# Performance work log

Measured on AMD Instinct MI355X. Metric: run time of the kernel, lower is better.

Reference implementation:

```python
import jax, jax.numpy as jnp
import numpy as np

N_NODES = 12288
N_EDGES = 393216  # N_NODES * avg_degree 32
IN_DIM, H1, H2 = 1433, 32, 16


def setup_inputs() -> dict:
    key = jax.random.key(0)
    ks = jax.random.split(key, 7)

    def glorot(k, fan_in, fan_out):
        r = np.sqrt(6.0 / (fan_in + fan_out)).astype(np.float32)
        return jax.random.uniform(k, (fan_in, fan_out), jnp.float32, -r, r)

    return {
        "X": jax.random.normal(ks[0], (N_NODES, IN_DIM), jnp.float32),
        "W1": glorot(ks[1], IN_DIM, H1),
        "W2": glorot(ks[2], H1, H1),
        "W3": glorot(ks[3], H1, H2),
        "edge_val": jax.random.uniform(ks[4], (N_EDGES,), jnp.float32),
        "edge_row": jax.random.randint(ks[5], (N_EDGES,), 0, N_NODES, jnp.int32),
        "edge_col": jax.random.randint(ks[6], (N_EDGES,), 0, N_NODES, jnp.int32),
    }


def reference(X, W1, W2, W3, edge_val, edge_row, edge_col):
    n = X.shape[0]

    def spmm(x):
        # sparse adj (COO) @ x : gather source rows, scale, scatter-add to dest
        return jax.ops.segment_sum(edge_val[:, None] * x[edge_col], edge_row, num_segments=n)

    h = jax.nn.relu(spmm(X @ W1))       # [N, 32]
    h = jax.nn.relu(spmm(h @ W2))       # [N, 32]
    Z = spmm(h @ W3)                    # [N, 16] (identity activation)
    A_pred = jax.nn.sigmoid(Z @ Z.T)    # [N, N] dot-product decode
    return (A_pred, Z)
```

## Files before the change

kernel.cpp:

```cpp
#include <hip/hip_runtime.h>


constexpr int NN = 12288;
constexpr int NE = 393216;
constexpr int KD = 1433;
constexpr int CAP = 96;

typedef float f32x4 __attribute__((ext_vector_type(4)));
typedef float f32x4u __attribute__((ext_vector_type(4), aligned(4)));
typedef float f32x16 __attribute__((ext_vector_type(16)));
typedef short shortx8 __attribute__((ext_vector_type(8)));

__device__ __forceinline__ unsigned short f2bf(float v) {
    unsigned int b = __float_as_uint(v);
    return (unsigned short)((b + 0x7FFFu + ((b >> 16) & 1u)) >> 16);
}

constexpr int KC = 256;
constexpr int NCH = 6;
constexpr int XST = KC + 8;
constexpr int G1B = (NN / 64) * NCH;

__global__ __launch_bounds__(256) void k_scatter_gemm1(const int* __restrict__ er,
                                                       const int* __restrict__ ec,
                                                       const float* __restrict__ ev,
                                                       int* __restrict__ cnt,
                                                       uint2* __restrict__ ebuf,
                                                       const float* __restrict__ X,
                                                       const float* __restrict__ W,
                                                       float* __restrict__ out) {
    if (blockIdx.x >= G1B) {
        int e = (blockIdx.x - G1B) * 256 + threadIdx.x;
        int r = er[e];
        int p = atomicAdd(&cnt[r], 1);
        if (p < CAP) ebuf[(size_t)r * CAP + p] = make_uint2((unsigned)ec[e], __float_as_uint(ev[e]));
        return;
    }
    __shared__ unsigned short wt[32 * XST];

    int rgB   = blockIdx.x / NCH;
    int chunk = blockIdx.x % NCH;
    int r0 = rgB * 64;
    int k0 = chunk * KC;
    int kt = min(KC, KD - k0);
    int nm = (kt + 15) >> 4;
    int t = threadIdx.x;

    int wtot = nm * 16 * 32;
    for (int e = t; e < wtot; e += 256) {
        int k = e >> 5, c = e & 31;
        float v = (k < kt) ? W[(size_t)(k0 + k) * 32 + c] : 0.f;
        wt[c * XST + k] = f2bf(v);
    }
    __syncthreads();

    int w = t >> 6, l = t & 63;
    int rg = w >> 1;
    int lr = l & 31, lh = l >> 5;
    int row = r0 + rg * 32 + lr;
    const float* xr = X + (size_t)row * KD + k0 + lh * 8;
    const unsigned short* wbase = wt + lr * XST + lh * 8;
    f32x16 acc = {0.f};
    for (int m = (w & 1); m < nm; m += 2) {
        int kk = m * 16 + lh * 8;
        float xv[8];
        if (kk + 8 <= kt) {
            f32x4u v0 = *(const f32x4u*)(xr + m * 16);
            f32x4u v1 = *(const f32x4u*)(xr + m * 16 + 4);
#pragma unroll
            for (int j = 0; j < 4; ++j) { xv[j] = v0[j]; xv[4 + j] = v1[j]; }
        } else {
#pragma unroll
            for (int j = 0; j < 8; ++j) xv[j] = (kk + j < kt) ? xr[m * 16 + j] : 0.f;
        }
        shortx8 a;
#pragma unroll
        for (int j = 0; j < 8; ++j) a[j] = (short)f2bf(xv[j]);
        shortx8 b = *(const shortx8*)(wbase + m * 16);
        acc = __builtin_amdgcn_mfma_f32_32x32x16_bf16(a, b, acc, 0, 0, 0);
    }
#pragma unroll
    for (int q = 0; q < 16; ++q) {
        int rf = (q & 3) + 8 * (q >> 2) + 4 * lh;
        atomicAdd(&out[(size_t)(r0 + rg * 32 + rf) * 32 + lr], acc[q]);
    }
}

template <int CO>
__global__ __launch_bounds__(256) void spmm_gemm(const float* __restrict__ in,
                                                 const float* __restrict__ Wm,
                                                 float* __restrict__ out,
                                                 const int* __restrict__ cnt,
                                                 const uint2* __restrict__ ebuf) {
    int tid = blockIdx.x * 256 + threadIdx.x;
    int r = tid >> 6;
    int lane = threadIdx.x & 63;
    int c = lane & 31, half = lane >> 5;
    int co = c & (CO - 1);
    float wcol[32];
#pragma unroll
    for (int k = 0; k < 32; ++k) wcol[k] = Wm[k * CO + co];
    int deg = min(cnt[r], CAP);
    int mid = (deg >> 1) & ~1;
    int lo = half ? mid : 0;
    int hi = half ? deg : mid;
    const uint2* eb2 = ebuf + (size_t)r * CAP;
    const uint4* eb4 = (const uint4*)eb2;
    float acc = 0.f;
    int i = lo;
#pragma unroll 2
    for (; i + 4 <= hi; i += 4) {
        uint4 e01 = eb4[i >> 1], e23 = eb4[(i >> 1) + 1];
        acc += __uint_as_float(e01.y) * in[(size_t)e01.x * 32 + c];
        acc += __uint_as_float(e01.w) * in[(size_t)e01.z * 32 + c];
        acc += __uint_as_float(e23.y) * in[(size_t)e23.x * 32 + c];
        acc += __uint_as_float(e23.w) * in[(size_t)e23.z * 32 + c];
    }
    for (; i < hi; ++i) {
        uint2 e = eb2[i];
        acc += __uint_as_float(e.y) * in[(size_t)e.x * 32 + c];
    }
    float h = fmaxf(acc + __shfl_xor(acc, 32), 0.f);
    float o = 0.f;
#pragma unroll
    for (int k = 0; k < 32; ++k)
        o += __shfl(h, (lane & 32) + k) * wcol[k];
    if (half == 0 && c < CO) out[(size_t)r * CO + co] = o;
}

__global__ __launch_bounds__(256) void spmm16(const float* __restrict__ in,
                                              float* __restrict__ out,
                                              unsigned short* __restrict__ zb,
                                              const int* __restrict__ cnt,
                                              const uint2* __restrict__ ebuf) {
    int tid = blockIdx.x * 256 + threadIdx.x;
    int r = tid >> 5;
    int sub = tid & 31;
    int c = sub & 15, half = sub >> 4;
    int deg = min(cnt[r], CAP);
    int mid = (deg >> 1) & ~1;
    int lo = half ? mid : 0;
    int hi = half ? deg : mid;
    const uint2* eb2 = ebuf + (size_t)r * CAP;
    const uint4* eb4 = (const uint4*)eb2;
    float acc = 0.f;
    int i = lo;
#pragma unroll 2
    for (; i + 4 <= hi; i += 4) {
        uint4 e01 = eb4[i >> 1], e23 = eb4[(i >> 1) + 1];
        acc += __uint_as_float(e01.y) * in[(size_t)e01.x * 16 + c];
        acc += __uint_as_float(e01.w) * in[(size_t)e01.z * 16 + c];
        acc += __uint_as_float(e23.y) * in[(size_t)e23.x * 16 + c];
        acc += __uint_as_float(e23.w) * in[(size_t)e23.z * 16 + c];
    }
    for (; i < hi; ++i) {
        uint2 e = eb2[i];
        acc += __uint_as_float(e.y) * in[(size_t)e.x * 16 + c];
    }
    float sv = acc + __shfl_xor(acc, 16);
    if (half == 0) {
        out[(size_t)r * 16 + c] = sv;
        zb[(size_t)r * 16 + c] = f2bf(sv);
    }
}

__global__ __launch_bounds__(256) void decode_mfma(const unsigned short* __restrict__ Zb,
                                                   float* __restrict__ A) {
    int id = blockIdx.x;
    int f = (id & 7) * (9216 / 8) + (id >> 3);
    int bi = f / 48, bj = f % 48;
    int w = threadIdx.x >> 6;
    int l = threadIdx.x & 63;
    int R = bi * 64;
    int C = bj * 256 + w * 64;
    int lr = l & 31, lh = l >> 5;

    shortx8 a0 = *(const shortx8*)(Zb + ((size_t)(R + lr) << 4) + lh * 8);
    shortx8 a1 = *(const shortx8*)(Zb + ((size_t)(R + 32 + lr) << 4) + lh * 8);
    shortx8 b0 = *(const shortx8*)(Zb + ((size_t)(C + lr) << 4) + lh * 8);
    shortx8 b1 = *(const shortx8*)(Zb + ((size_t)(C + 32 + lr) << 4) + lh * 8);

    f32x16 acc00 = {0.f}, acc01 = {0.f}, acc10 = {0.f}, acc11 = {0.f};
    acc00 = __builtin_amdgcn_mfma_f32_32x32x16_bf16(a0, b0, acc00, 0, 0, 0);
    acc01 = __builtin_amdgcn_mfma_f32_32x32x16_bf16(a0, b1, acc01, 0, 0, 0);
    acc10 = __builtin_amdgcn_mfma_f32_32x32x16_bf16(a1, b0, acc10, 0, 0, 0);
    acc11 = __builtin_amdgcn_mfma_f32_32x32x16_bf16(a1, b1, acc11, 0, 0, 0);

#pragma unroll
    for (int q = 0; q < 16; ++q) {
        int rf = (q & 3) + 8 * (q >> 2) + 4 * lh;
        float s00 = __fdividef(1.0f, 1.0f + __expf(-acc00[q]));
        float s01 = __fdividef(1.0f, 1.0f + __expf(-acc01[q]));
        float s10 = __fdividef(1.0f, 1.0f + __expf(-acc10[q]));
        float s11 = __fdividef(1.0f, 1.0f + __expf(-acc11[q]));
        __builtin_nontemporal_store(s00, &A[(size_t)(R + rf) * NN + C + lr]);
        __builtin_nontemporal_store(s01, &A[(size_t)(R + rf) * NN + C + 32 + lr]);
        __builtin_nontemporal_store(s10, &A[(size_t)(R + 32 + rf) * NN + C + lr]);
        __builtin_nontemporal_store(s11, &A[(size_t)(R + 32 + rf) * NN + C + 32 + lr]);
    }
}

extern "C" void kernel_launch(void* const* d_in, const int* in_sizes, int n_in,
                              void* d_out, int out_size, void* d_ws, size_t ws_size,
                              hipStream_t stream) {
    const float* X  = (const float*)d_in[0];
    const float* W1 = (const float*)d_in[1];
    const float* W2 = (const float*)d_in[2];
    const float* W3 = (const float*)d_in[3];
    const float* ev = (const float*)d_in[4];
    const int*   er = (const int*)d_in[5];
    const int*   ec = (const int*)d_in[6];

    float* A = (float*)d_out;
    float* Z = A + (size_t)NN * NN;

    int*   cnt = (int*)d_ws;
    float* t1 = (float*)(cnt + NN);
    float* t2 = t1 + (size_t)NN * 32;
    float* t3 = t2 + (size_t)NN * 32;
    unsigned short* Zb = (unsigned short*)t1;

    uint2* ebuf = (uint2*)(A + (size_t)140000000);

    (void)hipMemsetAsync(cnt, 0, NN * sizeof(int) + (size_t)NN * 32 * sizeof(float), stream);

    k_scatter_gemm1<<<G1B + NE / 256, 256, 0, stream>>>(er, ec, ev, cnt, ebuf, X, W1, t1);

    spmm_gemm<32><<<NN * 64 / 256, 256, 0, stream>>>(t1, W2, t2, cnt, ebuf);
    spmm_gemm<16><<<NN * 64 / 256, 256, 0, stream>>>(t2, W3, t3, cnt, ebuf);
    spmm16<<<NN * 32 / 256, 256, 0, stream>>>(t3, Z, Zb, cnt, ebuf);

    decode_mfma<<<192 * 48, 256, 0, stream>>>(Zb, A);
}
```

Baseline: 203.4 us.

## Split K across waves in-block and reduce via LDS instead of atomics

The first GEMM now gives each block 32 rows and has its four waves each take a quarter of the 1433-wide K dimension. Partial MFMA accumulators are summed in shared memory and written out with plain stores, replacing the global float atomics. Because no atomics accumulate into t1 any more, the output no longer needs zeroing and the memset is shortened. W1 is now read straight from global memory per lane rather than staged in LDS, which risks more and less-coalesced W traffic in exchange for dropping the staging pass and sync.

```diff
diff --git a/kernel.cpp b/kernel.cpp
--- a/kernel.cpp
+++ b/kernel.cpp
@@ -16,10 +16,9 @@
     return (unsigned short)((b + 0x7FFFu + ((b >> 16) & 1u)) >> 16);
 }
 
-constexpr int KC = 256;
-constexpr int NCH = 6;
-constexpr int XST = KC + 8;
-constexpr int G1B = (NN / 64) * NCH;
+constexpr int KQ = 368;
+constexpr int NMQ = 23;
+constexpr int G1B = NN / 32;
 
 __global__ __launch_bounds__(256) void k_scatter_gemm1(const int* __restrict__ er,
                                                        const int* __restrict__ ec,
@@ -36,53 +35,50 @@
         if (p < CAP) ebuf[(size_t)r * CAP + p] = make_uint2((unsigned)ec[e], __float_as_uint(ev[e]));
         return;
     }
-    __shared__ unsigned short wt[32 * XST];
-
-    int rgB   = blockIdx.x / NCH;
-    int chunk = blockIdx.x % NCH;
-    int r0 = rgB * 64;
-    int k0 = chunk * KC;
-    int kt = min(KC, KD - k0);
-    int nm = (kt + 15) >> 4;
+    __shared__ float cbuf[4][32 * 32];
+
+    int r0 = blockIdx.x * 32;
     int t = threadIdx.x;
-
-    int wtot = nm * 16 * 32;
-    for (int e = t; e < wtot; e += 256) {
-        int k = e >> 5, c = e & 31;
-        float v = (k < kt) ? W[(size_t)(k0 + k) * 32 + c] : 0.f;
-        wt[c * XST + k] = f2bf(v);
-    }
-    __syncthreads();
-
     int w = t >> 6, l = t & 63;
-    int rg = w >> 1;
     int lr = l & 31, lh = l >> 5;
-    int row = r0 + rg * 32 + lr;
-    const float* xr = X + (size_t)row * KD + k0 + lh * 8;
-    const unsigned short* wbase = wt + lr * XST + lh * 8;
+    int row = r0 + lr;
+    int qs = w * KQ;
+    const float* xr = X + (size_t)row * KD;
+
     f32x16 acc = {0.f};
-    for (int m = (w & 1); m < nm; m += 2) {
-        int kk = m * 16 + lh * 8;
+#pragma unroll 2
+    for (int m = 0; m < NMQ; ++m) {
+        int kk = qs + m * 16 + lh * 8;
         float xv[8];
-        if (kk + 8 <= kt) {
-            f32x4u v0 = *(const f32x4u*)(xr + m * 16);
-            f32x4u v1 = *(const f32x4u*)(xr + m * 16 + 4);
+        if (kk + 8 <= KD) {
+            f32x4u v0 = *(const f32x4u*)(xr + kk);
+            f32x4u v1 = *(const f32x4u*)(xr + kk + 4);
 #pragma unroll
             for (int j = 0; j < 4; ++j) { xv[j] = v0[j]; xv[4 + j] = v1[j]; }
         } else {
 #pragma unroll
-            for (int j = 0; j < 8; ++j) xv[j] = (kk + j < kt) ? xr[m * 16 + j] : 0.f;
+            for (int j = 0; j < 8; ++j) xv[j] = (kk + j < KD) ? xr[kk + j] : 0.f;
         }
-        shortx8 a;
-#pragma unroll
-        for (int j = 0; j < 8; ++j) a[j] = (short)f2bf(xv[j]);
-        shortx8 b = *(const shortx8*)(wbase + m * 16);
+        shortx8 a, b;
+#pragma unroll
+        for (int j = 0; j < 8; ++j) {
+            a[j] = (short)f2bf(xv[j]);
+            int kb = kk + j;
+            b[j] = (short)((kb < KD) ? f2bf(W[(size_t)kb * 32 + lr]) : 0);
+        }
         acc = __builtin_amdgcn_mfma_f32_32x32x16_bf16(a, b, acc, 0, 0, 0);
     }
 #pragma unroll
     for (int q = 0; q < 16; ++q) {
         int rf = (q & 3) + 8 * (q >> 2) + 4 * lh;
-        atomicAdd(&out[(size_t)(r0 + rg * 32 + rf) * 32 + lr], acc[q]);
+        cbuf[w][rf * 32 + lr] = acc[q];
+    }
+    __syncthreads();
+#pragma unroll
+    for (int it = 0; it < 4; ++it) {
+        int e = t + it * 256;
+        float v = cbuf[0][e] + cbuf[1][e] + cbuf[2][e] + cbuf[3][e];
+        out[(size_t)r0 * 32 + e] = v;
     }
 }
 
@@ -222,7 +218,7 @@
 
     uint2* ebuf = (uint2*)(A + (size_t)140000000);
 
-    (void)hipMemsetAsync(cnt, 0, NN * sizeof(int) + (size_t)NN * 32 * sizeof(float), stream);
+    (void)hipMemsetAsync(cnt, 0, NN * sizeof(int), stream);
 
     k_scatter_gemm1<<<G1B + NE / 256, 256, 0, stream>>>(er, ec, ev, cnt, ebuf, X, W1, t1);
 
```

After: 228.7 us. +12.5%, slower.
